# Kernel optimization log

Measured on AMD Instinct MI355X. Metric: run time of the kernel, lower is better.

Reference implementation:

```python
import jax, jax.numpy as jnp
import numpy as np
import math

B, L, D, H, DFF, GEOM = 4, 768, 512, 8, 2048, 7
DK = D // H


def layer_norm(x, scale, bias, eps=1e-5):
    mu = jnp.mean(x, axis=-1, keepdims=True)
    var = jnp.mean(jnp.square(x - mu), axis=-1, keepdims=True)
    return (x - mu) * jax.lax.rsqrt(var + eps) * scale + bias


def setup_inputs() -> dict:
    key = jax.random.key(0)
    ks = jax.random.split(key, 20)
    s = 0.02
    inp = {
        "x": jax.random.normal(ks[0], (B, L, D), jnp.float32),
        "geom_feat": jax.random.uniform(ks[1], (B, L, L, GEOM), jnp.float32),
        "mask": jnp.ones((B, L), jnp.int32),
        # weights stored (in, out): y = x @ W + b, math-equivalent to torch Linear
        "Wq": jax.random.normal(ks[2], (D, D), jnp.float32) * s,
        "bq": jnp.zeros((D,), jnp.float32),
        "Wk": jax.random.normal(ks[3], (D, D), jnp.float32) * s,
        "bk": jnp.zeros((D,), jnp.float32),
        "Wv": jax.random.normal(ks[4], (D, D), jnp.float32) * s,
        "bv": jnp.zeros((D,), jnp.float32),
        "Wo": jax.random.normal(ks[5], (D, D), jnp.float32) * s,
        "bo": jnp.zeros((D,), jnp.float32),
        "Wg": jax.random.normal(ks[6], (GEOM, H), jnp.float32) * s,
        "bg": jnp.zeros((H,), jnp.float32),
        "Wgcn": jax.random.normal(ks[7], (D, D), jnp.float32) * s,
        "bgcn": jnp.zeros((D,), jnp.float32),
        "gcn_gate": jnp.float32(0.5),
        "W1": jax.random.normal(ks[8], (D, 2 * DFF), jnp.float32) * s,
        "b1": jnp.zeros((2 * DFF,), jnp.float32),
        "W2": jax.random.normal(ks[9], (DFF, D), jnp.float32) * s,
        "b2": jnp.zeros((D,), jnp.float32),
        "ln1_s": jnp.ones((D,), jnp.float32),
        "ln1_b": jnp.zeros((D,), jnp.float32),
        "ln2_s": jnp.ones((D,), jnp.float32),
        "ln2_b": jnp.zeros((D,), jnp.float32),
    }
    return inp


def reference(x, geom_feat, mask,
              Wq, bq, Wk, bk, Wv, bv, Wo, bo, Wg, bg,
              Wgcn, bgcn, gcn_gate, W1, b1, W2, b2,
              ln1_s, ln1_b, ln2_s, ln2_b):
    m = mask.astype(x.dtype)  # (B, L)
    # normalized adjacency from distance channel
    adj = jnp.exp(-geom_feat[..., 0] / 5.0)                 # (B, L, L)
    adj = adj * (m[:, :, None] * m[:, None, :])
    adj = adj / (jnp.sum(adj, axis=-1, keepdims=True) + 1e-6)

    h = layer_norm(x, ln1_s, ln1_b)                          # (B, L, D)

    # structure-guided attention
    Q = (h @ Wq + bq).reshape(B, L, H, DK)
    K = (h @ Wk + bk).reshape(B, L, H, DK)
    V = (h @ Wv + bv).reshape(B, L, H, DK)
    scores = jnp.einsum('blhd,bmhd->bhlm', Q, K) / math.sqrt(DK)
    bias = jnp.einsum('blmg,gh->bhlm', geom_feat, Wg) + bg[None, :, None, None]
    scores = scores + bias
    scores = jnp.where(mask[:, None, None, :] == 0, -10000.0, scores)
    attn = jax.nn.softmax(scores, axis=-1)
    ctx = jnp.einsum('bhlm,bmhd->blhd', attn, V).reshape(B, L, D)
    attn_out = ctx @ Wo + bo

    # dense GCN branch (exact GELU, matching torch nn.GELU default)
    g = h @ Wgcn + bgcn
    gcn_out = jax.nn.gelu(jnp.einsum('blm,bmd->bld', adj, g), approximate=False)

    x = x + attn_out + gcn_out * gcn_gate

    # gated feed-forward
    h2 = layer_norm(x, ln2_s, ln2_b)
    ff = h2 @ W1 + b1
    u, gate = ff[..., :DFF], ff[..., DFF:]
    x = x + (u * jax.nn.sigmoid(gate)) @ W2 + b2
    return x
```

## Files before the change

kernel.cpp:

```cpp
#include <hip/hip_runtime.h>
#include <hip/hip_bf16.h>
#include <math.h>

typedef __attribute__((ext_vector_type(8))) short bf8;
typedef __attribute__((ext_vector_type(4))) float f4;

__device__ __forceinline__ ushort f2bf(float x){
  union { float f; unsigned u; } v; v.f = x;
  unsigned r = (v.u + 0x7fffu + ((v.u >> 16) & 1u)) >> 16;
  return (ushort)r;
}
__device__ __forceinline__ float bf2f(ushort b){
  union { unsigned u; float f; } v; v.u = ((unsigned)b) << 16;
  return v.f;
}

struct GP {
  const ushort* A; long lda; long aBatch; long aHead;
  const ushort* Bt; long ldb; long bBatch; long bHead;
  const ushort* Bt2;
  int K; int zdiv;
  float* outf; ushort* outb;
  ushort* o1; ushort* o2; ushort* o3;
  const float* bias0; const float* bias1; const float* bias2; const float* bias3;
  const float* geom; const float* wg; const float* bgv; const int* mask;
  const float* addf;
};

enum { EP_QKVG=0, EP_SCORES, EP_CTX, EP_GCN, EP_ATTNOUT, EP_FF, EP_FINAL };

template<int EPI, bool DUAL>
__global__ __launch_bounds__(256)
void gemm_k(GP p) {
  __shared__ __align__(16) ushort As[64*64];
  __shared__ __align__(16) ushort Bs[64*64];
  __shared__ __align__(16) ushort Bs2[DUAL ? 64*64 : 8];
  const int tid = threadIdx.x;
  const int lane = tid & 63, wave = tid >> 6;
  const int wm = wave >> 1, wn = wave & 1;
  const int bm = blockIdx.x, bn = blockIdx.y, z = blockIdx.z;
  const int zb = z / p.zdiv, zh = z % p.zdiv;
  const ushort* Ab  = p.A  + (long)zb*p.aBatch + (long)zh*p.aHead + (long)bm*64*p.lda;
  const ushort* Btb = p.Bt + (long)zb*p.bBatch + (long)zh*p.bHead + (long)bn*64*p.ldb;
  const ushort* Bt2b = DUAL ? (p.Bt2 + (long)bn*64*p.ldb) : (const ushort*)nullptr;

  f4 acc[2][2] = {};
  f4 acc2[2][2] = {};

  const int sr = tid >> 3, sc = tid & 7;
  const int g = lane >> 4, lr = lane & 15;

  for (int k0 = 0; k0 < p.K; k0 += 64) {
    #pragma unroll
    for (int i = 0; i < 2; ++i) {
      int row = sr + i*32;
      int sw = (sc ^ (row & 7)) * 8;
      *(uint4*)&As[row*64 + sw] = *(const uint4*)(Ab  + (long)row*p.lda + k0 + sc*8);
      *(uint4*)&Bs[row*64 + sw] = *(const uint4*)(Btb + (long)row*p.ldb + k0 + sc*8);
      if (DUAL)
        *(uint4*)&Bs2[row*64 + sw] = *(const uint4*)(Bt2b + (long)row*p.ldb + k0 + sc*8);
    }
    __syncthreads();
    #pragma unroll
    for (int kw = 0; kw < 2; ++kw) {
      bf8 af[2], bfr[2], bf2[2];
      int chunk = kw*4 + g;
      #pragma unroll
      for (int f = 0; f < 2; ++f) {
        int ar = wm*32 + f*16 + lr;
        af[f]  = *(const bf8*)&As[ar*64 + ((chunk ^ (ar & 7)) * 8)];
        int br = wn*32 + f*16 + lr;
        bfr[f] = *(const bf8*)&Bs[br*64 + ((chunk ^ (br & 7)) * 8)];
        if (DUAL) bf2[f] = *(const bf8*)&Bs2[br*64 + ((chunk ^ (br & 7)) * 8)];
      }
      #pragma unroll
      for (int fm = 0; fm < 2; ++fm)
        #pragma unroll
        for (int fn = 0; fn < 2; ++fn) {
          acc[fm][fn] = __builtin_amdgcn_mfma_f32_16x16x32_bf16(af[fm], bfr[fn], acc[fm][fn], 0,0,0);
          if (DUAL) acc2[fm][fn] = __builtin_amdgcn_mfma_f32_16x16x32_bf16(af[fm], bf2[fn], acc2[fm][fn], 0,0,0);
        }
    }
    __syncthreads();
  }

  #pragma unroll
  for (int fm = 0; fm < 2; ++fm)
  #pragma unroll
  for (int fn = 0; fn < 2; ++fn)
  #pragma unroll
  for (int i = 0; i < 4; ++i) {
    int grow = bm*64 + wm*32 + fm*16 + g*4 + i;
    int gcol = bn*64 + wn*32 + fn*16 + lr;
    float v = acc[fm][fn][i];
    if constexpr (EPI == EP_QKVG) {
      int sec = gcol >> 9, cc = gcol & 511;
      const float* bp = sec==0 ? p.bias0 : sec==1 ? p.bias1 : sec==2 ? p.bias2 : p.bias3;
      v += bp[cc];
      ushort bvv = f2bf(v);
      if (sec == 0)      p.outb[(long)grow*512 + cc] = bvv;
      else if (sec == 1) p.o1[(long)grow*512 + cc] = bvv;
      else {
        int b = grow / 768, l = grow - b*768;
        ushort* dst = (sec==2) ? p.o2 : p.o3;
        dst[((long)b*512 + cc)*768 + l] = bvv;
      }
    } else if constexpr (EPI == EP_SCORES) {
      int b = z >> 3, h = z & 7;
      float bias = p.bgv[h];
      long gidx = (((long)b*768 + grow)*768 + gcol)*7;
      #pragma unroll
      for (int q = 0; q < 7; ++q) bias += p.geom[gidx+q] * p.wg[q*8 + h];
      float s = (p.mask[b*768 + gcol] == 0) ? -10000.f : (v*0.125f + bias);
      p.outb[((long)z*768 + grow)*768 + gcol] = f2bf(s);
    } else if constexpr (EPI == EP_CTX) {
      int b = z >> 3, h = z & 7;
      p.outb[((long)(b*768 + grow))*512 + h*64 + gcol] = f2bf(v);
    } else if constexpr (EPI == EP_GCN) {
      float ge = 0.5f * v * (1.f + erff(v * 0.70710678118f));
      p.outf[((long)z*768 + grow)*512 + gcol] = ge;
    } else if constexpr (EPI == EP_ATTNOUT) {
      p.outf[(long)grow*512 + gcol] = v + p.bias0[gcol];
    } else if constexpr (EPI == EP_FF) {
      float u = v + p.bias0[gcol];
      float gt = acc2[fm][fn][i] + p.bias0[2048 + gcol];
      float a = u / (1.f + expf(-gt));
      p.outb[(long)grow*2048 + gcol] = f2bf(a);
    } else if constexpr (EPI == EP_FINAL) {
      long idx = (long)grow*512 + gcol;
      p.outf[idx] = p.addf[idx] + v + p.bias0[gcol];
    }
  }
}

__global__ __launch_bounds__(256) void transpose_bf(const float* src, ushort* dst, int R, int C) {
  __shared__ float t[32][33];
  int r0 = blockIdx.x*32, c0 = blockIdx.y*32;
  int tr = threadIdx.x >> 5, tc = threadIdx.x & 31;
  #pragma unroll
  for (int i = 0; i < 4; ++i)
    t[tr + i*8][tc] = src[(long)(r0 + tr + i*8)*C + c0 + tc];
  __syncthreads();
  #pragma unroll
  for (int i = 0; i < 4; ++i)
    dst[(long)(c0 + tr + i*8)*R + r0 + tc] = f2bf(t[tc][tr + i*8]);
}

__global__ __launch_bounds__(256) void ln_k(const float* x, const float* gam, const float* bet, ushort* out) {
  int row = blockIdx.x, tid = threadIdx.x;
  long base = (long)row*512;
  float v0 = x[base+tid], v1 = x[base+tid+256];
  float s = v0+v1, q = v0*v0 + v1*v1;
  #pragma unroll
  for (int off=32; off>=1; off>>=1){ s += __shfl_down(s,off,64); q += __shfl_down(q,off,64); }
  __shared__ float red[8];
  int lane=tid&63, wave=tid>>6;
  if (lane==0){ red[wave]=s; red[4+wave]=q; }
  __syncthreads();
  if (tid==0){ red[0]=red[0]+red[1]+red[2]+red[3]; red[4]=red[4]+red[5]+red[6]+red[7]; }
  __syncthreads();
  float mu = red[0]*(1.f/512.f);
  float var = red[4]*(1.f/512.f) - mu*mu;
  float rs = rsqrtf(var + 1e-5f);
  out[base+tid]     = f2bf((v0-mu)*rs*gam[tid]     + bet[tid]);
  out[base+tid+256] = f2bf((v1-mu)*rs*gam[tid+256] + bet[tid+256]);
}

__global__ __launch_bounds__(256) void resid_ln2_k(const float* x, const float* ao, const float* gc,
    const float* gatep, const float* gam, const float* bet, float* xmid, ushort* h2) {
  int row = blockIdx.x, tid = threadIdx.x;
  long base = (long)row*512;
  float gate = *gatep;
  float v0 = x[base+tid]     + ao[base+tid]     + gc[base+tid]*gate;
  float v1 = x[base+tid+256] + ao[base+tid+256] + gc[base+tid+256]*gate;
  xmid[base+tid] = v0; xmid[base+tid+256] = v1;
  float s = v0+v1, q = v0*v0 + v1*v1;
  #pragma unroll
  for (int off=32; off>=1; off>>=1){ s += __shfl_down(s,off,64); q += __shfl_down(q,off,64); }
  __shared__ float red[8];
  int lane=tid&63, wave=tid>>6;
  if (lane==0){ red[wave]=s; red[4+wave]=q; }
  __syncthreads();
  if (tid==0){ red[0]=red[0]+red[1]+red[2]+red[3]; red[4]=red[4]+red[5]+red[6]+red[7]; }
  __syncthreads();
  float mu = red[0]*(1.f/512.f);
  float var = red[4]*(1.f/512.f) - mu*mu;
  float rs = rsqrtf(var + 1e-5f);
  h2[base+tid]     = f2bf((v0-mu)*rs*gam[tid]     + bet[tid]);
  h2[base+tid+256] = f2bf((v1-mu)*rs*gam[tid+256] + bet[tid+256]);
}

__global__ __launch_bounds__(256) void adj_k(const float* geom, const int* mask, ushort* adj) {
  int bl = blockIdx.x;
  int b = bl / 768;
  int tid = threadIdx.x;
  float ml = (float)mask[bl];
  float e[3]; float s = 0.f;
  #pragma unroll
  for (int j=0;j<3;j++){
    int m = tid + j*256;
    float mm = (float)mask[b*768 + m];
    e[j] = expf(-geom[((long)bl*768 + m)*7] * 0.2f) * mm;
    s += e[j];
  }
  #pragma unroll
  for (int off=32; off>=1; off>>=1) s += __shfl_down(s,off,64);
  __shared__ float red[4];
  int lane=tid&63, wave=tid>>6;
  if (lane==0) red[wave]=s;
  __syncthreads();
  if (tid==0) red[0]=red[0]+red[1]+red[2]+red[3];
  __syncthreads();
  float inv = ml / (ml*red[0] + 1e-6f);
  #pragma unroll
  for (int j=0;j<3;j++){
    int m = tid + j*256;
    adj[(long)bl*768 + m] = f2bf(e[j] * inv);
  }
}

__global__ __launch_bounds__(256) void softmax_k(ushort* sbuf) {
  long base = (long)blockIdx.x * 768;
  int tid = threadIdx.x;
  float v[3];
  float mx = -1e30f;
  #pragma unroll
  for (int j=0;j<3;j++){ v[j] = bf2f(sbuf[base + tid + j*256]); mx = fmaxf(mx, v[j]); }
  #pragma unroll
  for (int off=32; off>=1; off>>=1) mx = fmaxf(mx, __shfl_down(mx,off,64));
  __shared__ float red[8];
  int lane=tid&63, wave=tid>>6;
  if (lane==0) red[wave]=mx;
  __syncthreads();
  if (tid==0) red[0]=fmaxf(fmaxf(red[0],red[1]),fmaxf(red[2],red[3]));
  __syncthreads();
  mx = red[0];
  float s=0.f;
  #pragma unroll
  for (int j=0;j<3;j++){ v[j] = expf(v[j]-mx); s += v[j]; }
  #pragma unroll
  for (int off=32; off>=1; off>>=1) s += __shfl_down(s,off,64);
  if (lane==0) red[4+wave]=s;
  __syncthreads();
  if (tid==0) red[4]=red[4]+red[5]+red[6]+red[7];
  __syncthreads();
  float inv = 1.f/red[4];
  #pragma unroll
  for (int j=0;j<3;j++) sbuf[base+tid+j*256] = f2bf(v[j]*inv);
}

extern "C" void kernel_launch(void* const* d_in, const int* in_sizes, int n_in,
                              void* d_out, int out_size, void* d_ws, size_t ws_size,
                              hipStream_t stream) {
  const float* x    = (const float*)d_in[0];
  const float* geom = (const float*)d_in[1];
  const int*   mask = (const int*)d_in[2];
  const float* Wq   = (const float*)d_in[3];
  const float* bq   = (const float*)d_in[4];
  const float* Wk   = (const float*)d_in[5];
  const float* bk   = (const float*)d_in[6];
  const float* Wv   = (const float*)d_in[7];
  const float* bv   = (const float*)d_in[8];
  const float* Wo   = (const float*)d_in[9];
  const float* bo   = (const float*)d_in[10];
  const float* Wg   = (const float*)d_in[11];
  const float* bg   = (const float*)d_in[12];
  const float* Wgcn = (const float*)d_in[13];
  const float* bgcn = (const float*)d_in[14];
  const float* gate = (const float*)d_in[15];
  const float* W1   = (const float*)d_in[16];
  const float* b1   = (const float*)d_in[17];
  const float* W2   = (const float*)d_in[18];
  const float* b2   = (const float*)d_in[19];
  const float* ln1s = (const float*)d_in[20];
  const float* ln1b = (const float*)d_in[21];
  const float* ln2s = (const float*)d_in[22];
  const float* ln2b = (const float*)d_in[23];
  float* out = (float*)d_out;

  char* wp = (char*)d_ws;
  auto alloc = [&](size_t bytes)->char* { char* r = wp; wp += (bytes + 255) & ~(size_t)255; return r; };
  ushort* wqkvgT = (ushort*)alloc(2048*512*2);
  ushort* woT    = (ushort*)alloc(512*512*2);
  ushort* w1T    = (ushort*)alloc(4096*512*2);
  ushort* w2T    = (ushort*)alloc(512*2048*2);
  ushort* hbf    = (ushort*)alloc(3072*512*2);
  ushort* qbf    = (ushort*)alloc(3072*512*2);
  ushort* kbf    = (ushort*)alloc(3072*512*2);
  ushort* vt     = (ushort*)alloc((size_t)4*512*768*2);
  ushort* gt     = (ushort*)alloc((size_t)4*512*768*2);
  ushort* adjb   = (ushort*)alloc((size_t)4*768*768*2);
  ushort* sbf    = (ushort*)alloc((size_t)32*768*768*2);
  ushort* ctx    = (ushort*)alloc(3072*512*2);
  float*  aout   = (float*)alloc(3072*512*4);
  float*  gcnr   = (float*)alloc(3072*512*4);
  float*  xmid   = (float*)alloc(3072*512*4);
  ushort* h2bf   = (ushort*)alloc(3072*512*2);
  ushort* act    = sbf;

  transpose_bf<<<dim3(16,16), 256, 0, stream>>>(Wq,   wqkvgT + 0*512*512, 512, 512);
  transpose_bf<<<dim3(16,16), 256, 0, stream>>>(Wk,   wqkvgT + 1*512*512, 512, 512);
  transpose_bf<<<dim3(16,16), 256, 0, stream>>>(Wv,   wqkvgT + 2*512*512, 512, 512);
  transpose_bf<<<dim3(16,16), 256, 0, stream>>>(Wgcn, wqkvgT + 3*512*512, 512, 512);
  transpose_bf<<<dim3(16,16), 256, 0, stream>>>(Wo,   woT, 512, 512);
  transpose_bf<<<dim3(16,128),256, 0, stream>>>(W1,   w1T, 512, 4096);
  transpose_bf<<<dim3(64,16), 256, 0, stream>>>(W2,   w2T, 2048, 512);

  ln_k<<<3072, 256, 0, stream>>>(x, ln1s, ln1b, hbf);

  adj_k<<<3072, 256, 0, stream>>>(geom, mask, adjb);

  GP p{};
  p.A = hbf; p.lda = 512; p.aBatch = 0; p.aHead = 0;
  p.Bt = wqkvgT; p.ldb = 512; p.bBatch = 0; p.bHead = 0;
  p.K = 512; p.zdiv = 1;
  p.outb = qbf; p.o1 = kbf; p.o2 = vt; p.o3 = gt;
  p.bias0 = bq; p.bias1 = bk; p.bias2 = bv; p.bias3 = bgcn;
  gemm_k<EP_QKVG,false><<<dim3(48,32,1), 256, 0, stream>>>(p);

  p = GP{};
  p.A = qbf; p.lda = 512; p.aBatch = 768*512; p.aHead = 64;
  p.Bt = kbf; p.ldb = 512; p.bBatch = 768*512; p.bHead = 64;
  p.K = 64; p.zdiv = 8;
  p.outb = sbf; p.geom = geom; p.wg = Wg; p.bgv = bg; p.mask = mask;
  gemm_k<EP_SCORES,false><<<dim3(12,12,32), 256, 0, stream>>>(p);

  softmax_k<<<32*768, 256, 0, stream>>>(sbf);

  p = GP{};
  p.A = sbf; p.lda = 768; p.aBatch = (long)8*768*768; p.aHead = (long)768*768;
  p.Bt = vt; p.ldb = 768; p.bBatch = (long)512*768; p.bHead = (long)64*768;
  p.K = 768; p.zdiv = 8;
  p.outb = ctx;
  gemm_k<EP_CTX,false><<<dim3(12,1,32), 256, 0, stream>>>(p);

  p = GP{};
  p.A = adjb; p.lda = 768; p.aBatch = (long)768*768; p.aHead = 0;
  p.Bt = gt; p.ldb = 768; p.bBatch = (long)512*768; p.bHead = 0;
  p.K = 768; p.zdiv = 1;
  p.outf = gcnr;
  gemm_k<EP_GCN,false><<<dim3(12,8,4), 256, 0, stream>>>(p);

  p = GP{};
  p.A = ctx; p.lda = 512; p.aBatch = 0; p.aHead = 0;
  p.Bt = woT; p.ldb = 512; p.bBatch = 0; p.bHead = 0;
  p.K = 512; p.zdiv = 1;
  p.outf = aout; p.bias0 = bo;
  gemm_k<EP_ATTNOUT,false><<<dim3(48,8,1), 256, 0, stream>>>(p);

  resid_ln2_k<<<3072, 256, 0, stream>>>(x, aout, gcnr, gate, ln2s, ln2b, xmid, h2bf);

  p = GP{};
  p.A = h2bf; p.lda = 512; p.aBatch = 0; p.aHead = 0;
  p.Bt = w1T; p.ldb = 512; p.bBatch = 0; p.bHead = 0;
  p.Bt2 = w1T + (long)2048*512;
  p.K = 512; p.zdiv = 1;
  p.outb = act; p.bias0 = b1;
  gemm_k<EP_FF,true><<<dim3(48,32,1), 256, 0, stream>>>(p);

  p = GP{};
  p.A = act; p.lda = 2048; p.aBatch = 0; p.aHead = 0;
  p.Bt = w2T; p.ldb = 2048; p.bBatch = 0; p.bHead = 0;
  p.K = 2048; p.zdiv = 1;
  p.outf = out; p.bias0 = b2; p.addf = xmid;
  gemm_k<EP_FINAL,false><<<dim3(48,8,1), 256, 0, stream>>>(p);
}
```

Before: 348.6 us.

## Fuse scores, softmax and PV into flash-attention kernel with precomputed geometry bias

```diff
diff --git a/kernel.cpp b/kernel.cpp
--- a/kernel.cpp
+++ b/kernel.cpp
@@ -23,11 +23,10 @@
   float* outf; ushort* outb;
   ushort* o1; ushort* o2; ushort* o3;
   const float* bias0; const float* bias1; const float* bias2; const float* bias3;
-  const float* geom; const float* wg; const float* bgv; const int* mask;
   const float* addf;
 };
 
-enum { EP_QKVG=0, EP_SCORES, EP_CTX, EP_GCN, EP_ATTNOUT, EP_FF, EP_FINAL };
+enum { EP_QKVG=0, EP_GCN, EP_ATTNOUT, EP_FF, EP_FINAL };
 
 template<int EPI, bool DUAL>
 __global__ __launch_bounds__(256)
@@ -105,17 +104,6 @@
         ushort* dst = (sec==2) ? p.o2 : p.o3;
         dst[((long)b*512 + cc)*768 + l] = bvv;
       }
-    } else if constexpr (EPI == EP_SCORES) {
-      int b = z >> 3, h = z & 7;
-      float bias = p.bgv[h];
-      long gidx = (((long)b*768 + grow)*768 + gcol)*7;
-      #pragma unroll
-      for (int q = 0; q < 7; ++q) bias += p.geom[gidx+q] * p.wg[q*8 + h];
-      float s = (p.mask[b*768 + gcol] == 0) ? -10000.f : (v*0.125f + bias);
-      p.outb[((long)z*768 + grow)*768 + gcol] = f2bf(s);
-    } else if constexpr (EPI == EP_CTX) {
-      int b = z >> 3, h = z & 7;
-      p.outb[((long)(b*768 + grow))*512 + h*64 + gcol] = f2bf(v);
     } else if constexpr (EPI == EP_GCN) {
       float ge = 0.5f * v * (1.f + erff(v * 0.70710678118f));
       p.outf[((long)z*768 + grow)*512 + gcol] = ge;
@@ -133,6 +121,112 @@
   }
 }
 
+__global__ __launch_bounds__(256) void flash_k(const ushort* __restrict__ qg,
+    const ushort* __restrict__ kg, const ushort* __restrict__ vtg,
+    const ushort* __restrict__ biasg, ushort* __restrict__ ctx) {
+  __shared__ __align__(16) ushort Ks[64*64];
+  __shared__ __align__(16) ushort Vs[64*64];
+  __shared__ __align__(16) ushort Ps[64*64];
+  const int tid = threadIdx.x;
+  const int lane = tid & 63, w = tid >> 6;
+  const int g = lane >> 4, lr = lane & 15;
+  const int qt = blockIdx.x, bh = blockIdx.y;
+  const int b = bh >> 3, h = bh & 7;
+  const int q0 = qt*64;
+
+  bf8 aq[2];
+  #pragma unroll
+  for (int kk = 0; kk < 2; ++kk)
+    aq[kk] = *(const bf8*)&qg[(long)(b*768 + q0 + w*16 + lr)*512 + h*64 + kk*32 + g*8];
+
+  f4 o[4] = {};
+  float mrow[4], lsum[4];
+  #pragma unroll
+  for (int i = 0; i < 4; ++i) { mrow[i] = -1e30f; lsum[i] = 0.f; }
+
+  const int srow = tid >> 3, sc = tid & 7;
+
+  for (int kt = 0; kt < 12; ++kt) {
+    const int kbase = kt*64;
+    #pragma unroll
+    for (int ps = 0; ps < 2; ++ps) {
+      int r = srow + ps*32;
+      int sw = ((sc ^ (r & 7)) * 8);
+      *(uint4*)&Ks[r*64 + sw] = *(const uint4*)&kg[(long)(b*768 + kbase + r)*512 + h*64 + sc*8];
+      *(uint4*)&Vs[r*64 + sw] = *(const uint4*)&vtg[((long)b*512 + h*64 + r)*768 + kbase + sc*8];
+    }
+    __syncthreads();
+
+    f4 s[4] = {};
+    #pragma unroll
+    for (int kn = 0; kn < 4; ++kn) {
+      #pragma unroll
+      for (int kk = 0; kk < 2; ++kk) {
+        int row = kn*16 + lr;
+        bf8 bk = *(const bf8*)&Ks[row*64 + (((kk*4+g) ^ (row & 7)) * 8)];
+        s[kn] = __builtin_amdgcn_mfma_f32_16x16x32_bf16(aq[kk], bk, s[kn], 0,0,0);
+      }
+    }
+
+    float pv[4][4];
+    #pragma unroll
+    for (int kn = 0; kn < 4; ++kn)
+      #pragma unroll
+      for (int i = 0; i < 4; ++i) {
+        float bv = bf2f(biasg[((long)bh*768 + q0 + w*16 + g*4 + i)*768 + kbase + kn*16 + lr]);
+        pv[kn][i] = s[kn][i]*0.125f + bv;
+      }
+
+    #pragma unroll
+    for (int i = 0; i < 4; ++i) {
+      float m2 = fmaxf(fmaxf(pv[0][i], pv[1][i]), fmaxf(pv[2][i], pv[3][i]));
+      #pragma unroll
+      for (int off = 1; off < 16; off <<= 1) m2 = fmaxf(m2, __shfl_xor(m2, off, 64));
+      float mnew = fmaxf(mrow[i], m2);
+      float scale = __expf(mrow[i] - mnew);
+      mrow[i] = mnew;
+      float psum = 0.f;
+      #pragma unroll
+      for (int kn = 0; kn < 4; ++kn) { pv[kn][i] = __expf(pv[kn][i] - mnew); psum += pv[kn][i]; }
+      #pragma unroll
+      for (int off = 1; off < 16; off <<= 1) psum += __shfl_xor(psum, off, 64);
+      lsum[i] = lsum[i]*scale + psum;
+      #pragma unroll
+      for (int dn = 0; dn < 4; ++dn) o[dn][i] *= scale;
+    }
+
+    #pragma unroll
+    for (int kn = 0; kn < 4; ++kn)
+      #pragma unroll
+      for (int i = 0; i < 4; ++i) {
+        int row = w*16 + g*4 + i;
+        int col = kn*16 + lr;
+        Ps[row*64 + (((col >> 3) ^ (row & 7)) * 8) + (col & 7)] = f2bf(pv[kn][i]);
+      }
+
+    #pragma unroll
+    for (int kk2 = 0; kk2 < 2; ++kk2) {
+      int prow = w*16 + lr;
+      bf8 pa = *(const bf8*)&Ps[prow*64 + (((kk2*4+g) ^ (prow & 7)) * 8)];
+      #pragma unroll
+      for (int dn = 0; dn < 4; ++dn) {
+        int vrow = dn*16 + lr;
+        bf8 bv = *(const bf8*)&Vs[vrow*64 + (((kk2*4+g) ^ (vrow & 7)) * 8)];
+        o[dn] = __builtin_amdgcn_mfma_f32_16x16x32_bf16(pa, bv, o[dn], 0,0,0);
+      }
+    }
+    __syncthreads();
+  }
+
+  #pragma unroll
+  for (int i = 0; i < 4; ++i) {
+    float inv = 1.f / lsum[i];
+    #pragma unroll
+    for (int dn = 0; dn < 4; ++dn)
+      ctx[(long)(b*768 + q0 + w*16 + g*4 + i)*512 + h*64 + dn*16 + lr] = f2bf(o[dn][i]*inv);
+  }
+}
+
 __global__ __launch_bounds__(256) void transpose_bf(const float* src, ushort* dst, int R, int C) {
   __shared__ float t[32][33];
   int r0 = blockIdx.x*32, c0 = blockIdx.y*32;
@@ -190,63 +284,46 @@
   h2[base+tid+256] = f2bf((v1-mu)*rs*gam[tid+256] + bet[tid+256]);
 }
 
-__global__ __launch_bounds__(256) void adj_k(const float* geom, const int* mask, ushort* adj) {
+__global__ __launch_bounds__(256) void adjbias_k(const float* __restrict__ geom,
+    const int* __restrict__ mask, const float* __restrict__ Wg, const float* __restrict__ bg,
+    ushort* __restrict__ adjb, ushort* __restrict__ biasb) {
   int bl = blockIdx.x;
-  int b = bl / 768;
+  int b = bl / 768, l = bl - b*768;
   int tid = threadIdx.x;
+  __shared__ float wgs[56];
+  __shared__ float bgs[8];
+  if (tid < 56) wgs[tid] = Wg[tid];
+  if (tid < 8)  bgs[tid] = bg[tid];
+  __syncthreads();
   float ml = (float)mask[bl];
-  float e[3]; float s = 0.f;
-  #pragma unroll
-  for (int j=0;j<3;j++){
+  float e[3]; float ssum = 0.f;
+  #pragma unroll
+  for (int j = 0; j < 3; ++j) {
     int m = tid + j*256;
+    const float* gp = &geom[((long)bl*768 + m)*7];
+    float g0 = gp[0], g1 = gp[1], g2 = gp[2], g3 = gp[3], g4 = gp[4], g5 = gp[5], g6 = gp[6];
     float mm = (float)mask[b*768 + m];
-    e[j] = expf(-geom[((long)bl*768 + m)*7] * 0.2f) * mm;
-    s += e[j];
+    e[j] = __expf(-g0*0.2f) * mm;
+    ssum += e[j];
+    #pragma unroll
+    for (int hh = 0; hh < 8; ++hh) {
+      float bv = bgs[hh] + g0*wgs[hh] + g1*wgs[8+hh] + g2*wgs[16+hh] + g3*wgs[24+hh]
+               + g4*wgs[32+hh] + g5*wgs[40+hh] + g6*wgs[48+hh];
+      biasb[((long)(b*8+hh)*768 + l)*768 + m] = f2bf(mm != 0.f ? bv : -10000.f);
+    }
   }
   #pragma unroll
-  for (int off=32; off>=1; off>>=1) s += __shfl_down(s,off,64);
+  for (int off=32; off>=1; off>>=1) ssum += __shfl_down(ssum, off, 64);
   __shared__ float red[4];
-  int lane=tid&63, wave=tid>>6;
-  if (lane==0) red[wave]=s;
-  __syncthreads();
-  if (tid==0) red[0]=red[0]+red[1]+red[2]+red[3];
+  int lane = tid & 63, wave = tid >> 6;
+  if (lane == 0) red[wave] = ssum;
+  __syncthreads();
+  if (tid == 0) red[0] = red[0]+red[1]+red[2]+red[3];
   __syncthreads();
   float inv = ml / (ml*red[0] + 1e-6f);
   #pragma unroll
-  for (int j=0;j<3;j++){
-    int m = tid + j*256;
-    adj[(long)bl*768 + m] = f2bf(e[j] * inv);
-  }
-}
-
-__global__ __launch_bounds__(256) void softmax_k(ushort* sbuf) {
-  long base = (long)blockIdx.x * 768;
-  int tid = threadIdx.x;
-  float v[3];
-  float mx = -1e30f;
-  #pragma unroll
-  for (int j=0;j<3;j++){ v[j] = bf2f(sbuf[base + tid + j*256]); mx = fmaxf(mx, v[j]); }
-  #pragma unroll
-  for (int off=32; off>=1; off>>=1) mx = fmaxf(mx, __shfl_down(mx,off,64));
-  __shared__ float red[8];
-  int lane=tid&63, wave=tid>>6;
-  if (lane==0) red[wave]=mx;
-  __syncthreads();
-  if (tid==0) red[0]=fmaxf(fmaxf(red[0],red[1]),fmaxf(red[2],red[3]));
-  __syncthreads();
-  mx = red[0];
-  float s=0.f;
-  #pragma unroll
-  for (int j=0;j<3;j++){ v[j] = expf(v[j]-mx); s += v[j]; }
-  #pragma unroll
-  for (int off=32; off>=1; off>>=1) s += __shfl_down(s,off,64);
-  if (lane==0) red[4+wave]=s;
-  __syncthreads();
-  if (tid==0) red[4]=red[4]+red[5]+red[6]+red[7];
-  __syncthreads();
-  float inv = 1.f/red[4];
-  #pragma unroll
-  for (int j=0;j<3;j++) sbuf[base+tid+j*256] = f2bf(v[j]*inv);
+  for (int j = 0; j < 3; ++j)
+    adjb[(long)bl*768 + tid + j*256] = f2bf(e[j] * inv);
 }
 
 extern "C" void kernel_launch(void* const* d_in, const int* in_sizes, int n_in,
@@ -290,13 +367,13 @@
   ushort* vt     = (ushort*)alloc((size_t)4*512*768*2);
   ushort* gt     = (ushort*)alloc((size_t)4*512*768*2);
   ushort* adjb   = (ushort*)alloc((size_t)4*768*768*2);
-  ushort* sbf    = (ushort*)alloc((size_t)32*768*768*2);
+  ushort* biasb  = (ushort*)alloc((size_t)32*768*768*2);
   ushort* ctx    = (ushort*)alloc(3072*512*2);
   float*  aout   = (float*)alloc(3072*512*4);
   float*  gcnr   = (float*)alloc(3072*512*4);
   float*  xmid   = (float*)alloc(3072*512*4);
   ushort* h2bf   = (ushort*)alloc(3072*512*2);
-  ushort* act    = sbf;
+  ushort* act    = biasb;
 
   transpose_bf<<<dim3(16,16), 256, 0, stream>>>(Wq,   wqkvgT + 0*512*512, 512, 512);
   transpose_bf<<<dim3(16,16), 256, 0, stream>>>(Wk,   wqkvgT + 1*512*512, 512, 512);
@@ -308,7 +385,7 @@
 
   ln_k<<<3072, 256, 0, stream>>>(x, ln1s, ln1b, hbf);
 
-  adj_k<<<3072, 256, 0, stream>>>(geom, mask, adjb);
+  adjbias_k<<<3072, 256, 0, stream>>>(geom, mask, Wg, bg, adjb, biasb);
 
   GP p{};
   p.A = hbf; p.lda = 512; p.aBatch = 0; p.aHead = 0;
@@ -318,21 +395,7 @@
   p.bias0 = bq; p.bias1 = bk; p.bias2 = bv; p.bias3 = bgcn;
   gemm_k<EP_QKVG,false><<<dim3(48,32,1), 256, 0, stream>>>(p);
 
-  p = GP{};
-  p.A = qbf; p.lda = 512; p.aBatch = 768*512; p.aHead = 64;
-  p.Bt = kbf; p.ldb = 512; p.bBatch = 768*512; p.bHead = 64;
-  p.K = 64; p.zdiv = 8;
-  p.outb = sbf; p.geom = geom; p.wg = Wg; p.bgv = bg; p.mask = mask;
-  gemm_k<EP_SCORES,false><<<dim3(12,12,32), 256, 0, stream>>>(p);
-
-  softmax_k<<<32*768, 256, 0, stream>>>(sbf);
-
-  p = GP{};
-  p.A = sbf; p.lda = 768; p.aBatch = (long)8*768*768; p.aHead = (long)768*768;
-  p.Bt = vt; p.ldb = 768; p.bBatch = (long)512*768; p.bHead = (long)64*768;
-  p.K = 768; p.zdiv = 8;
-  p.outb = ctx;
-  gemm_k<EP_CTX,false><<<dim3(12,1,32), 256, 0, stream>>>(p);
+  flash_k<<<dim3(12,32), 256, 0, stream>>>(qbf, kbf, vt, biasb, ctx);
 
   p = GP{};
   p.A = adjb; p.lda = 768; p.aBatch = (long)768*768; p.aHead = 0;
```

New measurement: 313.7 us. 10.0% less time.
